# Optimization experiments

Measured on AMD Instinct MI355X. Metric: run time of the kernel, lower is better.

The kernel has to match this reference:

```python
import jax, jax.numpy as jnp
import numpy as np

H, W = 192, 640
MAX_ITERS = 200
EPS = 1e-8


def setup_inputs() -> dict:
    key = jax.random.key(0)
    k1, k2 = jax.random.split(key)
    B = 16
    ptcloud = jax.random.normal(k1, (B, 3, H * W), dtype=jnp.float32)
    # KITTI-like intrinsics; cy = 96 so the ground prior starts at row 96.
    Kmat = jnp.tile(
        jnp.array([[721.5, 0.0, 320.0], [0.0, 721.5, 96.0], [0.0, 0.0, 1.0]],
                  dtype=jnp.float32)[None], (B, 1, 1))
    ys = 96
    xs, xe = W * 3 // 8, W * 5 // 8
    n_prior = (H - ys) * (xe - xs)  # 15360
    sample_idx = jax.random.randint(k2, (MAX_ITERS, 3), 0, n_prior, dtype=jnp.int32)
    return {"ptcloud": ptcloud, "K": Kmat, "sample_idx": sample_idx}


def _median_low(x):
    """torch.median semantics (lower middle element), x: (B, N) -> (B, 1)."""
    n = x.shape[1]
    s = jnp.sort(x, axis=1)
    m = (n - 1) // 2
    return s[:, m:m + 1]


def _mad_threshold(y):
    med = _median_low(y)                       # (B, 1)
    return _median_low(jnp.abs(med - y))       # (B, 1)


def _ransac_plane(prior, sample_idx, thr):
    """prior: (B, N, 3), sample_idx: (I, 3), thr: (B, 1) -> plane (B, 4)."""
    samples = prior[:, sample_idx]             # (B, I, 3, 3)
    p1, p2, p3 = samples[:, :, 0], samples[:, :, 1], samples[:, :, 2]
    n = jnp.cross(p2 - p1, p3 - p1)            # (B, I, 3)
    n = n / (jnp.linalg.norm(n, axis=-1, keepdims=True) + EPS)
    d = -jnp.sum(n * p1, axis=-1)              # (B, I)
    # point-plane distances for all prior points: (B, I, N)
    dist = jnp.abs(jnp.einsum('bnc,bic->bin', prior, n) + d[:, :, None])
    counts = jnp.sum(dist <= thr[:, :, None], axis=-1)  # (B, I)
    best = jnp.argmax(counts, axis=1)                    # (B,)
    plane = jnp.concatenate([n, d[..., None]], axis=-1)  # (B, I, 4)
    return jnp.take_along_axis(plane, best[:, None, None], axis=1)[:, 0]


def reference(ptcloud, K, sample_idx):
    B = ptcloud.shape[0]
    # ground prior region (static slice; K is concrete at trace time here)
    ys = int(K[:, 1, 2].mean())
    xs, xe = W * 3 // 8, W * 5 // 8
    pc = ptcloud.reshape(B, 3, H, W)
    prior = pc[:, :, ys:, xs:xe].reshape(B, 3, -1).transpose(0, 2, 1)  # (B, N, 3)
    thr = _mad_threshold(prior[..., 1])                                # (B, 1)
    plane = _ransac_plane(prior, sample_idx, thr)                      # (B, 4)
    pts_all = ptcloud.transpose(0, 2, 1)                               # (B, M, 3)
    dist_all = jnp.abs(jnp.einsum('bmc,bc->bm', pts_all, plane[:, :3]) + plane[:, 3:4])
    inlier_mask = (dist_all <= thr).reshape(B, H, W)
    return plane, inlier_mask
```

## Files before the change

kernel.cpp:

```cpp
#include <hip/hip_runtime.h>
#include <cstdint>

#define HW      122880
#define NPRIOR  15360
#define NITER   200
#define NB      16
#define RANKSEL 7680u
#define NBINS   8192
#define LISTCAP 2048

__device__ __forceinline__ uint32_t f2k(float f) {
  uint32_t u = __float_as_uint(f);
  return (u & 0x80000000u) ? ~u : (u ^ 0x80000000u);
}
__device__ __forceinline__ float k2f(uint32_t k) {
  uint32_t u = (k & 0x80000000u) ? (k ^ 0x80000000u) : ~k;
  return __uint_as_float(u);
}

__device__ uint32_t select13(uint32_t* __restrict__ keys, uint32_t* __restrict__ hist,
                             uint32_t* __restrict__ wpart, uint32_t* __restrict__ res,
                             uint32_t* __restrict__ list, uint32_t* __restrict__ pcnt,
                             uint32_t* __restrict__ pfin, int tid) {
  {
    uint4 z = {0u, 0u, 0u, 0u};
    ((uint4*)hist)[tid] = z;
    ((uint4*)hist)[1024 + tid] = z;
  }
  if (tid == 0) *pcnt = 0u;
  __syncthreads();
#pragma unroll
  for (int j = 0; j < 15; j++) {
    uint32_t k = keys[j * 1024 + tid];
    atomicAdd(&hist[k >> 19], 1u);
  }
  __syncthreads();
  uint32_t h[8];
  uint32_t s = 0u;
#pragma unroll
  for (int e = 0; e < 8; e++) {
    h[e] = hist[8 * tid + e];
    s += h[e];
  }
  uint32_t incl = s;
#pragma unroll
  for (int off = 1; off < 64; off <<= 1) {
    uint32_t n = __shfl_up(incl, off);
    if ((tid & 63) >= off) incl += n;
  }
  if ((tid & 63) == 63) wpart[tid >> 6] = incl;
  __syncthreads();
  {
    uint32_t base = 0u;
    const int wv = tid >> 6;
#pragma unroll
    for (int w = 0; w < 16; w++) base += (w < wv) ? wpart[w] : 0u;
    incl += base;
  }
  const uint32_t excl = incl - s;
  if (RANKSEL > excl && RANKSEL <= incl) {
    uint32_t c = excl;
#pragma unroll
    for (int e = 0; e < 8; e++) {
      uint32_t nc = c + h[e];
      if (RANKSEL > c && RANKSEL <= nc) {
        res[0] = (uint32_t)(8 * tid + e);
        res[1] = RANKSEL - c;
      }
      c = nc;
    }
  }
  __syncthreads();
  const uint32_t bin = res[0];
  const uint32_t tp = res[1];
#pragma unroll
  for (int j = 0; j < 15; j++) {
    uint32_t k = keys[j * 1024 + tid];
    if ((k >> 19) == bin) {
      uint32_t p = atomicAdd(pcnt, 1u);
      if (p < LISTCAP) list[p] = k & 0x7FFFFu;
    }
  }
  __syncthreads();
  if (tid < 64) {
    const uint32_t n = *pcnt;
    uint32_t kk[8];
#pragma unroll
    for (int j = 0; j < 8; j++) {
      uint32_t p = (uint32_t)tid + 64u * j;
      kk[j] = (p < n) ? list[p] : 0xFFFFFFFFu;
    }
    uint32_t lo = 0u, hi = 0x7FFFFu;
    while (lo < hi) {
      uint32_t mid = lo + ((hi - lo) >> 1);
      int c = 0;
#pragma unroll
      for (int j = 0; j < 8; j++) c += (kk[j] <= mid) ? 1 : 0;
      for (uint32_t p = 512u + (uint32_t)tid; p < n; p += 64u)
        c += (list[p] <= mid) ? 1 : 0;
#pragma unroll
      for (int off = 32; off; off >>= 1) c += __shfl_down(c, off);
      c = __shfl(c, 0);
      if ((uint32_t)c >= tp) hi = mid; else lo = mid + 1u;
    }
    if (tid == 0) *pfin = (bin << 19) | lo;
  }
  __syncthreads();
  return *pfin;
}

__global__ __launch_bounds__(1024, 4)
void thr_kernel(const float* __restrict__ pt, const int* __restrict__ sidx,
                float* __restrict__ thr_out, float* __restrict__ planes,
                uint32_t* __restrict__ bestkey) {
  __shared__ uint32_t keys[NPRIOR];
  __shared__ uint32_t hist[NBINS];
  __shared__ uint32_t list[LISTCAP];
  __shared__ uint32_t wpart[16];
  __shared__ uint32_t res[2];
  __shared__ uint32_t lcnt;
  __shared__ uint32_t fin;
  const int b = blockIdx.x;
  const int tid = threadIdx.x;
  if (tid == 0) bestkey[b] = 0u;

  if (tid < NITER) {
    const float* base = pt + (size_t)b * 3 * HW;
    float p[3][3];
#pragma unroll
    for (int k = 0; k < 3; k++) {
      int s = sidx[tid * 3 + k];
      int r = s / 160;
      int c = s - r * 160;
      int hw = (96 + r) * 640 + 240 + c;
      p[k][0] = base[hw];
      p[k][1] = base[HW + hw];
      p[k][2] = base[2 * HW + hw];
    }
    float ux = __fsub_rn(p[1][0], p[0][0]);
    float uy = __fsub_rn(p[1][1], p[0][1]);
    float uz = __fsub_rn(p[1][2], p[0][2]);
    float vx = __fsub_rn(p[2][0], p[0][0]);
    float vy = __fsub_rn(p[2][1], p[0][1]);
    float vz = __fsub_rn(p[2][2], p[0][2]);
    float nx = __fsub_rn(__fmul_rn(uy, vz), __fmul_rn(uz, vy));
    float ny = __fsub_rn(__fmul_rn(uz, vx), __fmul_rn(ux, vz));
    float nz = __fsub_rn(__fmul_rn(ux, vy), __fmul_rn(uy, vx));
    float nn = __fsqrt_rn(__fadd_rn(__fadd_rn(__fmul_rn(nx, nx), __fmul_rn(ny, ny)),
                                    __fmul_rn(nz, nz)));
    float den = __fadd_rn(nn, 1e-8f);
    nx = __fdiv_rn(nx, den);
    ny = __fdiv_rn(ny, den);
    nz = __fdiv_rn(nz, den);
    float s3 = __fadd_rn(__fadd_rn(__fmul_rn(nx, p[0][0]), __fmul_rn(ny, p[0][1])),
                         __fmul_rn(nz, p[0][2]));
    int t = b * NITER + tid;
    planes[4 * t + 0] = nx;
    planes[4 * t + 1] = ny;
    planes[4 * t + 2] = nz;
    planes[4 * t + 3] = -s3;
  }

  const float* ybase = pt + (size_t)b * 3 * HW + HW;
#pragma unroll
  for (int j = 0; j < 15; j++) {
    int i = j * 1024 + tid;
    int r = i / 160;
    int c = i - r * 160;
    keys[j * 1024 + tid] = f2k(ybase[(96 + r) * 640 + 240 + c]);
  }
  uint32_t medk = select13(keys, hist, wpart, res, list, &lcnt, &fin, tid);
  float med = k2f(medk);

#pragma unroll
  for (int j = 0; j < 15; j++) {
    float y = k2f(keys[j * 1024 + tid]);
    keys[j * 1024 + tid] = __float_as_uint(fabsf(__fsub_rn(med, y)));
  }
  uint32_t thk = select13(keys, hist, wpart, res, list, &lcnt, &fin, tid);
  if (tid == 0) thr_out[b] = __uint_as_float(thk);
}

__global__ __launch_bounds__(256)
void count_kernel(const float* __restrict__ pt, const float* __restrict__ planes,
                  const float* __restrict__ thr_arr, uint32_t* __restrict__ bestkey) {
  const int chunk = blockIdx.x;
  const int b = blockIdx.y;
  const int tid = threadIdx.x;
  __shared__ int cnt_s[13];
  if (tid < 13) cnt_s[tid] = 0;
  __syncthreads();
  const int p0 = chunk * 13;
  float plr[13][4];
#pragma unroll
  for (int k = 0; k < 13; k++) {
    int pidx = p0 + k;
    if (pidx < NITER) {
      const float* pp = planes + (size_t)(b * NITER + pidx) * 4;
      plr[k][0] = pp[0]; plr[k][1] = pp[1]; plr[k][2] = pp[2]; plr[k][3] = pp[3];
    } else {
      plr[k][0] = plr[k][1] = plr[k][2] = plr[k][3] = 0.0f;
    }
  }
  const float thr = thr_arr[b];
  const float* base = pt + (size_t)b * 3 * HW;
  int cnt[13];
#pragma unroll
  for (int k = 0; k < 13; k++) cnt[k] = 0;
  for (int ii = 0; ii < NPRIOR; ii += 1024) {
    int i = ii + tid * 4;
    int r = i / 160;
    int c = i - r * 160;
    int hw = (96 + r) * 640 + 240 + c;
    float4 x4 = *(const float4*)(base + hw);
    float4 y4 = *(const float4*)(base + HW + hw);
    float4 z4 = *(const float4*)(base + 2 * HW + hw);
    float xs[4] = {x4.x, x4.y, x4.z, x4.w};
    float ys[4] = {y4.x, y4.y, y4.z, y4.w};
    float zs[4] = {z4.x, z4.y, z4.z, z4.w};
#pragma unroll
    for (int q = 0; q < 4; q++) {
      float x = xs[q], y = ys[q], z = zs[q];
#pragma unroll
      for (int k = 0; k < 13; k++) {
        float s = __fadd_rn(__fadd_rn(__fmul_rn(x, plr[k][0]), __fmul_rn(y, plr[k][1])),
                            __fmul_rn(z, plr[k][2]));
        float dist = fabsf(__fadd_rn(s, plr[k][3]));
        cnt[k] += (dist <= thr) ? 1 : 0;
      }
    }
  }
#pragma unroll
  for (int k = 0; k < 13; k++) {
    int v = cnt[k];
#pragma unroll
    for (int off = 32; off; off >>= 1) v += __shfl_down(v, off);
    if ((tid & 63) == 0) atomicAdd(&cnt_s[k], v);
  }
  __syncthreads();
  if (tid < 13 && p0 + tid < NITER) {
    int iter = p0 + tid;
    uint32_t key = ((uint32_t)cnt_s[tid] << 8) | (uint32_t)(255 - iter);
    atomicMax(&bestkey[b], key);
  }
}

__global__ __launch_bounds__(256)
void mask_kernel(const float* __restrict__ pt, const float* __restrict__ planes,
                 const float* __restrict__ thr_arr, const uint32_t* __restrict__ bestkey,
                 float* __restrict__ out) {
  const int g4 = (blockIdx.x * 256 + threadIdx.x) * 4;
  const int b = g4 / HW;
  const int m = g4 - b * HW;
  const int best = 255 - (int)(bestkey[b] & 255u);
  const float* plane = planes + (size_t)(b * NITER + best) * 4;
  const float nx = plane[0], ny = plane[1], nz = plane[2], dd = plane[3];
  const float thr = thr_arr[b];
  const float* base = pt + (size_t)b * 3 * HW;
  float4 x4 = *(const float4*)(base + m);
  float4 y4 = *(const float4*)(base + HW + m);
  float4 z4 = *(const float4*)(base + 2 * HW + m);
  float xs[4] = {x4.x, x4.y, x4.z, x4.w};
  float ys[4] = {y4.x, y4.y, y4.z, y4.w};
  float zs[4] = {z4.x, z4.y, z4.z, z4.w};
  float4 o;
  float* os = (float*)&o;
#pragma unroll
  for (int q = 0; q < 4; q++) {
    float s = __fadd_rn(__fadd_rn(__fmul_rn(xs[q], nx), __fmul_rn(ys[q], ny)),
                        __fmul_rn(zs[q], nz));
    float dist = fabsf(__fadd_rn(s, dd));
    os[q] = (dist <= thr) ? 1.0f : 0.0f;
  }
  *(float4*)(out + 64 + (size_t)g4) = o;
  if (m == 0) {
#pragma unroll
    for (int q = 0; q < 4; q++) out[b * 4 + q] = plane[q];
  }
}

extern "C" void kernel_launch(void* const* d_in, const int* in_sizes, int n_in,
                              void* d_out, int out_size, void* d_ws, size_t ws_size,
                              hipStream_t stream) {
  (void)in_sizes; (void)n_in; (void)out_size; (void)ws_size;
  const float* pt = (const float*)d_in[0];
  const int* sidx = (const int*)d_in[2];
  float* out = (float*)d_out;

  float* thr      = (float*)d_ws;
  float* planes   = thr + 16;
  uint32_t* bkey  = (uint32_t*)(planes + NB * NITER * 4);

  thr_kernel<<<NB, 1024, 0, stream>>>(pt, sidx, thr, planes, bkey);
  count_kernel<<<dim3(16, NB), 256, 0, stream>>>(pt, planes, thr, bkey);
  mask_kernel<<<(NB * HW) / 1024, 256, 0, stream>>>(pt, planes, thr, bkey, out);
}
```

Baseline: 119.0 us.

## Fuse threshold, count, and mask stages into one cooperative kernel with grid sync

Replaces the three separate launches with a single cooperative kernel of 256 blocks that uses grid-wide syncs between the threshold/plane stage, the RANSAC count stage and the mask stage. The median selection now runs with 256 threads and rereads y values from global memory instead of keeping keys in shared memory. Plane generation is spread across 200 blocks, with one plane per batch computed by each thread. The aim is to cut launch gaps and the serial tail of a 16-block threshold kernel, at the cost of grid.sync overhead and a threshold stage with fewer threads per batch.

```diff
diff --git a/kernel.cpp b/kernel.cpp
--- a/kernel.cpp
+++ b/kernel.cpp
@@ -1,5 +1,8 @@
 #include <hip/hip_runtime.h>
+#include <hip/hip_cooperative_groups.h>
 #include <cstdint>
+
+namespace cg = cooperative_groups;
 
 #define HW      122880
 #define NPRIOR  15360
@@ -18,29 +21,39 @@
   return __uint_as_float(u);
 }
 
-__device__ uint32_t select13(uint32_t* __restrict__ keys, uint32_t* __restrict__ hist,
-                             uint32_t* __restrict__ wpart, uint32_t* __restrict__ res,
-                             uint32_t* __restrict__ list, uint32_t* __restrict__ pcnt,
-                             uint32_t* __restrict__ pfin, int tid) {
+__device__ uint32_t select256(const float* __restrict__ ybase, int tid,
+                              bool pass2, float med, uint32_t* __restrict__ hist,
+                              uint32_t* __restrict__ list, uint32_t* __restrict__ wpart,
+                              uint32_t* __restrict__ res, uint32_t* __restrict__ pcnt,
+                              uint32_t* __restrict__ pfin) {
   {
     uint4 z = {0u, 0u, 0u, 0u};
-    ((uint4*)hist)[tid] = z;
-    ((uint4*)hist)[1024 + tid] = z;
+#pragma unroll
+    for (int j = 0; j < 8; j++) ((uint4*)hist)[tid + j * 256] = z;
   }
   if (tid == 0) *pcnt = 0u;
   __syncthreads();
 #pragma unroll
   for (int j = 0; j < 15; j++) {
-    uint32_t k = keys[j * 1024 + tid];
-    atomicAdd(&hist[k >> 19], 1u);
-  }
-  __syncthreads();
-  uint32_t h[8];
+    int i = tid * 4 + j * 1024;
+    int r = i / 160;
+    int c = i - r * 160;
+    float4 v = *(const float4*)(ybase + (96 + r) * 640 + 240 + c);
+    float vs[4] = {v.x, v.y, v.z, v.w};
+#pragma unroll
+    for (int e = 0; e < 4; e++) {
+      uint32_t k = pass2 ? __float_as_uint(fabsf(__fsub_rn(med, vs[e]))) : f2k(vs[e]);
+      atomicAdd(&hist[k >> 19], 1u);
+    }
+  }
+  __syncthreads();
+  uint32_t h[32];
   uint32_t s = 0u;
 #pragma unroll
-  for (int e = 0; e < 8; e++) {
-    h[e] = hist[8 * tid + e];
-    s += h[e];
+  for (int j = 0; j < 8; j++) {
+    uint4 q = ((const uint4*)hist)[8 * tid + j];
+    h[4 * j + 0] = q.x; h[4 * j + 1] = q.y; h[4 * j + 2] = q.z; h[4 * j + 3] = q.w;
+    s += q.x + q.y + q.z + q.w;
   }
   uint32_t incl = s;
 #pragma unroll
@@ -54,17 +67,17 @@
     uint32_t base = 0u;
     const int wv = tid >> 6;
 #pragma unroll
-    for (int w = 0; w < 16; w++) base += (w < wv) ? wpart[w] : 0u;
+    for (int w = 0; w < 4; w++) base += (w < wv) ? wpart[w] : 0u;
     incl += base;
   }
   const uint32_t excl = incl - s;
   if (RANKSEL > excl && RANKSEL <= incl) {
     uint32_t c = excl;
 #pragma unroll
-    for (int e = 0; e < 8; e++) {
+    for (int e = 0; e < 32; e++) {
       uint32_t nc = c + h[e];
       if (RANKSEL > c && RANKSEL <= nc) {
-        res[0] = (uint32_t)(8 * tid + e);
+        res[0] = (uint32_t)(32 * tid + e);
         res[1] = RANKSEL - c;
       }
       c = nc;
@@ -75,10 +88,18 @@
   const uint32_t tp = res[1];
 #pragma unroll
   for (int j = 0; j < 15; j++) {
-    uint32_t k = keys[j * 1024 + tid];
-    if ((k >> 19) == bin) {
-      uint32_t p = atomicAdd(pcnt, 1u);
-      if (p < LISTCAP) list[p] = k & 0x7FFFFu;
+    int i = tid * 4 + j * 1024;
+    int r = i / 160;
+    int c = i - r * 160;
+    float4 v = *(const float4*)(ybase + (96 + r) * 640 + 240 + c);
+    float vs[4] = {v.x, v.y, v.z, v.w};
+#pragma unroll
+    for (int e = 0; e < 4; e++) {
+      uint32_t k = pass2 ? __float_as_uint(fabsf(__fsub_rn(med, vs[e]))) : f2k(vs[e]);
+      if ((k >> 19) == bin) {
+        uint32_t p = atomicAdd(pcnt, 1u);
+        if (p < LISTCAP) list[p] = k & 0x7FFFFu;
+      }
     }
   }
   __syncthreads();
@@ -109,173 +130,163 @@
   return *pfin;
 }
 
-__global__ __launch_bounds__(1024, 4)
-void thr_kernel(const float* __restrict__ pt, const int* __restrict__ sidx,
-                float* __restrict__ thr_out, float* __restrict__ planes,
-                uint32_t* __restrict__ bestkey) {
-  __shared__ uint32_t keys[NPRIOR];
+__global__ __launch_bounds__(256)
+void fused_kernel(const float* __restrict__ pt, const int* __restrict__ sidx,
+                  float* __restrict__ thr_arr, float* __restrict__ planes,
+                  uint32_t* __restrict__ bestkey, float* __restrict__ out) {
   __shared__ uint32_t hist[NBINS];
   __shared__ uint32_t list[LISTCAP];
-  __shared__ uint32_t wpart[16];
+  __shared__ uint32_t wpart[4];
   __shared__ uint32_t res[2];
-  __shared__ uint32_t lcnt;
-  __shared__ uint32_t fin;
-  const int b = blockIdx.x;
+  __shared__ uint32_t pcnt, pfin;
+  __shared__ int cnt_s[13];
+  cg::grid_group grid = cg::this_grid();
+  const int g = blockIdx.x;
   const int tid = threadIdx.x;
-  if (tid == 0) bestkey[b] = 0u;
-
-  if (tid < NITER) {
+
+  if (g < NB) {
+    const int b = g;
+    const float* ybase = pt + (size_t)b * 3 * HW + HW;
+    uint32_t medk = select256(ybase, tid, false, 0.0f, hist, list, wpart, res, &pcnt, &pfin);
+    float med = k2f(medk);
+    uint32_t thk = select256(ybase, tid, true, med, hist, list, wpart, res, &pcnt, &pfin);
+    if (tid == 0) thr_arr[b] = __uint_as_float(thk);
+  } else if (g < 16 + NITER) {
+    const int i = g - 16;
+    if (tid < NB) {
+      const int b = tid;
+      const float* base = pt + (size_t)b * 3 * HW;
+      float p[3][3];
+#pragma unroll
+      for (int k = 0; k < 3; k++) {
+        int s = sidx[i * 3 + k];
+        int r = s / 160;
+        int c = s - r * 160;
+        int hw = (96 + r) * 640 + 240 + c;
+        p[k][0] = base[hw];
+        p[k][1] = base[HW + hw];
+        p[k][2] = base[2 * HW + hw];
+      }
+      float ux = __fsub_rn(p[1][0], p[0][0]);
+      float uy = __fsub_rn(p[1][1], p[0][1]);
+      float uz = __fsub_rn(p[1][2], p[0][2]);
+      float vx = __fsub_rn(p[2][0], p[0][0]);
+      float vy = __fsub_rn(p[2][1], p[0][1]);
+      float vz = __fsub_rn(p[2][2], p[0][2]);
+      float nx = __fsub_rn(__fmul_rn(uy, vz), __fmul_rn(uz, vy));
+      float ny = __fsub_rn(__fmul_rn(uz, vx), __fmul_rn(ux, vz));
+      float nz = __fsub_rn(__fmul_rn(ux, vy), __fmul_rn(uy, vx));
+      float nn = __fsqrt_rn(__fadd_rn(__fadd_rn(__fmul_rn(nx, nx), __fmul_rn(ny, ny)),
+                                      __fmul_rn(nz, nz)));
+      float den = __fadd_rn(nn, 1e-8f);
+      nx = __fdiv_rn(nx, den);
+      ny = __fdiv_rn(ny, den);
+      nz = __fdiv_rn(nz, den);
+      float s3 = __fadd_rn(__fadd_rn(__fmul_rn(nx, p[0][0]), __fmul_rn(ny, p[0][1])),
+                           __fmul_rn(nz, p[0][2]));
+      int t = b * NITER + i;
+      planes[4 * t + 0] = nx;
+      planes[4 * t + 1] = ny;
+      planes[4 * t + 2] = nz;
+      planes[4 * t + 3] = -s3;
+    }
+  } else if (g == 16 + NITER) {
+    if (tid < NB) bestkey[tid] = 0u;
+  }
+  grid.sync();
+
+  {
+    const int b = g >> 4;
+    const int chunk = g & 15;
+    if (tid < 13) cnt_s[tid] = 0;
+    __syncthreads();
+    const int p0 = chunk * 13;
+    float plr[13][4];
+#pragma unroll
+    for (int k = 0; k < 13; k++) {
+      int pidx = p0 + k;
+      if (pidx < NITER) {
+        const float* pp = planes + (size_t)(b * NITER + pidx) * 4;
+        plr[k][0] = pp[0]; plr[k][1] = pp[1]; plr[k][2] = pp[2]; plr[k][3] = pp[3];
+      } else {
+        plr[k][0] = plr[k][1] = plr[k][2] = plr[k][3] = 0.0f;
+      }
+    }
+    const float thr = thr_arr[b];
     const float* base = pt + (size_t)b * 3 * HW;
-    float p[3][3];
-#pragma unroll
-    for (int k = 0; k < 3; k++) {
-      int s = sidx[tid * 3 + k];
-      int r = s / 160;
-      int c = s - r * 160;
+    int cnt[13];
+#pragma unroll
+    for (int k = 0; k < 13; k++) cnt[k] = 0;
+    for (int ii = 0; ii < NPRIOR; ii += 1024) {
+      int i = ii + tid * 4;
+      int r = i / 160;
+      int c = i - r * 160;
       int hw = (96 + r) * 640 + 240 + c;
-      p[k][0] = base[hw];
-      p[k][1] = base[HW + hw];
-      p[k][2] = base[2 * HW + hw];
-    }
-    float ux = __fsub_rn(p[1][0], p[0][0]);
-    float uy = __fsub_rn(p[1][1], p[0][1]);
-    float uz = __fsub_rn(p[1][2], p[0][2]);
-    float vx = __fsub_rn(p[2][0], p[0][0]);
-    float vy = __fsub_rn(p[2][1], p[0][1]);
-    float vz = __fsub_rn(p[2][2], p[0][2]);
-    float nx = __fsub_rn(__fmul_rn(uy, vz), __fmul_rn(uz, vy));
-    float ny = __fsub_rn(__fmul_rn(uz, vx), __fmul_rn(ux, vz));
-    float nz = __fsub_rn(__fmul_rn(ux, vy), __fmul_rn(uy, vx));
-    float nn = __fsqrt_rn(__fadd_rn(__fadd_rn(__fmul_rn(nx, nx), __fmul_rn(ny, ny)),
-                                    __fmul_rn(nz, nz)));
-    float den = __fadd_rn(nn, 1e-8f);
-    nx = __fdiv_rn(nx, den);
-    ny = __fdiv_rn(ny, den);
-    nz = __fdiv_rn(nz, den);
-    float s3 = __fadd_rn(__fadd_rn(__fmul_rn(nx, p[0][0]), __fmul_rn(ny, p[0][1])),
-                         __fmul_rn(nz, p[0][2]));
-    int t = b * NITER + tid;
-    planes[4 * t + 0] = nx;
-    planes[4 * t + 1] = ny;
-    planes[4 * t + 2] = nz;
-    planes[4 * t + 3] = -s3;
-  }
-
-  const float* ybase = pt + (size_t)b * 3 * HW + HW;
-#pragma unroll
-  for (int j = 0; j < 15; j++) {
-    int i = j * 1024 + tid;
-    int r = i / 160;
-    int c = i - r * 160;
-    keys[j * 1024 + tid] = f2k(ybase[(96 + r) * 640 + 240 + c]);
-  }
-  uint32_t medk = select13(keys, hist, wpart, res, list, &lcnt, &fin, tid);
-  float med = k2f(medk);
-
-#pragma unroll
-  for (int j = 0; j < 15; j++) {
-    float y = k2f(keys[j * 1024 + tid]);
-    keys[j * 1024 + tid] = __float_as_uint(fabsf(__fsub_rn(med, y)));
-  }
-  uint32_t thk = select13(keys, hist, wpart, res, list, &lcnt, &fin, tid);
-  if (tid == 0) thr_out[b] = __uint_as_float(thk);
-}
-
-__global__ __launch_bounds__(256)
-void count_kernel(const float* __restrict__ pt, const float* __restrict__ planes,
-                  const float* __restrict__ thr_arr, uint32_t* __restrict__ bestkey) {
-  const int chunk = blockIdx.x;
-  const int b = blockIdx.y;
-  const int tid = threadIdx.x;
-  __shared__ int cnt_s[13];
-  if (tid < 13) cnt_s[tid] = 0;
-  __syncthreads();
-  const int p0 = chunk * 13;
-  float plr[13][4];
-#pragma unroll
-  for (int k = 0; k < 13; k++) {
-    int pidx = p0 + k;
-    if (pidx < NITER) {
-      const float* pp = planes + (size_t)(b * NITER + pidx) * 4;
-      plr[k][0] = pp[0]; plr[k][1] = pp[1]; plr[k][2] = pp[2]; plr[k][3] = pp[3];
-    } else {
-      plr[k][0] = plr[k][1] = plr[k][2] = plr[k][3] = 0.0f;
-    }
-  }
-  const float thr = thr_arr[b];
-  const float* base = pt + (size_t)b * 3 * HW;
-  int cnt[13];
-#pragma unroll
-  for (int k = 0; k < 13; k++) cnt[k] = 0;
-  for (int ii = 0; ii < NPRIOR; ii += 1024) {
-    int i = ii + tid * 4;
-    int r = i / 160;
-    int c = i - r * 160;
-    int hw = (96 + r) * 640 + 240 + c;
-    float4 x4 = *(const float4*)(base + hw);
-    float4 y4 = *(const float4*)(base + HW + hw);
-    float4 z4 = *(const float4*)(base + 2 * HW + hw);
+      float4 x4 = *(const float4*)(base + hw);
+      float4 y4 = *(const float4*)(base + HW + hw);
+      float4 z4 = *(const float4*)(base + 2 * HW + hw);
+      float xs[4] = {x4.x, x4.y, x4.z, x4.w};
+      float ys[4] = {y4.x, y4.y, y4.z, y4.w};
+      float zs[4] = {z4.x, z4.y, z4.z, z4.w};
+#pragma unroll
+      for (int q = 0; q < 4; q++) {
+        float x = xs[q], y = ys[q], z = zs[q];
+#pragma unroll
+        for (int k = 0; k < 13; k++) {
+          float s = __fadd_rn(__fadd_rn(__fmul_rn(x, plr[k][0]), __fmul_rn(y, plr[k][1])),
+                              __fmul_rn(z, plr[k][2]));
+          float dist = fabsf(__fadd_rn(s, plr[k][3]));
+          cnt[k] += (dist <= thr) ? 1 : 0;
+        }
+      }
+    }
+#pragma unroll
+    for (int k = 0; k < 13; k++) {
+      int v = cnt[k];
+#pragma unroll
+      for (int off = 32; off; off >>= 1) v += __shfl_down(v, off);
+      if ((tid & 63) == 0) atomicAdd(&cnt_s[k], v);
+    }
+    __syncthreads();
+    if (tid < 13 && p0 + tid < NITER) {
+      int iter = p0 + tid;
+      uint32_t key = ((uint32_t)cnt_s[tid] << 8) | (uint32_t)(255 - iter);
+      atomicMax(&bestkey[b], key);
+    }
+  }
+  grid.sync();
+
+  for (uint32_t u = (uint32_t)g * 256u + (uint32_t)tid; u < (uint32_t)(NB * HW / 4);
+       u += 65536u) {
+    const int g4 = (int)u * 4;
+    const int b = g4 / HW;
+    const int m = g4 - b * HW;
+    const int best = 255 - (int)(bestkey[b] & 255u);
+    const float* plane = planes + (size_t)(b * NITER + best) * 4;
+    const float nx = plane[0], ny = plane[1], nz = plane[2], dd = plane[3];
+    const float thr = thr_arr[b];
+    const float* base = pt + (size_t)b * 3 * HW;
+    float4 x4 = *(const float4*)(base + m);
+    float4 y4 = *(const float4*)(base + HW + m);
+    float4 z4 = *(const float4*)(base + 2 * HW + m);
     float xs[4] = {x4.x, x4.y, x4.z, x4.w};
     float ys[4] = {y4.x, y4.y, y4.z, y4.w};
     float zs[4] = {z4.x, z4.y, z4.z, z4.w};
+    float4 o;
+    float* os = (float*)&o;
 #pragma unroll
     for (int q = 0; q < 4; q++) {
-      float x = xs[q], y = ys[q], z = zs[q];
-#pragma unroll
-      for (int k = 0; k < 13; k++) {
-        float s = __fadd_rn(__fadd_rn(__fmul_rn(x, plr[k][0]), __fmul_rn(y, plr[k][1])),
-                            __fmul_rn(z, plr[k][2]));
-        float dist = fabsf(__fadd_rn(s, plr[k][3]));
-        cnt[k] += (dist <= thr) ? 1 : 0;
-      }
-    }
-  }
-#pragma unroll
-  for (int k = 0; k < 13; k++) {
-    int v = cnt[k];
-#pragma unroll
-    for (int off = 32; off; off >>= 1) v += __shfl_down(v, off);
-    if ((tid & 63) == 0) atomicAdd(&cnt_s[k], v);
-  }
-  __syncthreads();
-  if (tid < 13 && p0 + tid < NITER) {
-    int iter = p0 + tid;
-    uint32_t key = ((uint32_t)cnt_s[tid] << 8) | (uint32_t)(255 - iter);
-    atomicMax(&bestkey[b], key);
-  }
-}
-
-__global__ __launch_bounds__(256)
-void mask_kernel(const float* __restrict__ pt, const float* __restrict__ planes,
-                 const float* __restrict__ thr_arr, const uint32_t* __restrict__ bestkey,
-                 float* __restrict__ out) {
-  const int g4 = (blockIdx.x * 256 + threadIdx.x) * 4;
-  const int b = g4 / HW;
-  const int m = g4 - b * HW;
-  const int best = 255 - (int)(bestkey[b] & 255u);
-  const float* plane = planes + (size_t)(b * NITER + best) * 4;
-  const float nx = plane[0], ny = plane[1], nz = plane[2], dd = plane[3];
-  const float thr = thr_arr[b];
-  const float* base = pt + (size_t)b * 3 * HW;
-  float4 x4 = *(const float4*)(base + m);
-  float4 y4 = *(const float4*)(base + HW + m);
-  float4 z4 = *(const float4*)(base + 2 * HW + m);
-  float xs[4] = {x4.x, x4.y, x4.z, x4.w};
-  float ys[4] = {y4.x, y4.y, y4.z, y4.w};
-  float zs[4] = {z4.x, z4.y, z4.z, z4.w};
-  float4 o;
-  float* os = (float*)&o;
-#pragma unroll
-  for (int q = 0; q < 4; q++) {
-    float s = __fadd_rn(__fadd_rn(__fmul_rn(xs[q], nx), __fmul_rn(ys[q], ny)),
-                        __fmul_rn(zs[q], nz));
-    float dist = fabsf(__fadd_rn(s, dd));
-    os[q] = (dist <= thr) ? 1.0f : 0.0f;
-  }
-  *(float4*)(out + 64 + (size_t)g4) = o;
-  if (m == 0) {
-#pragma unroll
-    for (int q = 0; q < 4; q++) out[b * 4 + q] = plane[q];
+      float s = __fadd_rn(__fadd_rn(__fmul_rn(xs[q], nx), __fmul_rn(ys[q], ny)),
+                          __fmul_rn(zs[q], nz));
+      float dist = fabsf(__fadd_rn(s, dd));
+      os[q] = (dist <= thr) ? 1.0f : 0.0f;
+    }
+    *(float4*)(out + 64 + (size_t)g4) = o;
+  }
+  if (g == 0 && tid < 64) {
+    const int b = tid >> 2;
+    const int best = 255 - (int)(bestkey[b] & 255u);
+    out[tid] = planes[(size_t)(b * NITER + best) * 4 + (tid & 3)];
   }
 }
 
@@ -291,7 +302,8 @@
   float* planes   = thr + 16;
   uint32_t* bkey  = (uint32_t*)(planes + NB * NITER * 4);
 
-  thr_kernel<<<NB, 1024, 0, stream>>>(pt, sidx, thr, planes, bkey);
-  count_kernel<<<dim3(16, NB), 256, 0, stream>>>(pt, planes, thr, bkey);
-  mask_kernel<<<(NB * HW) / 1024, 256, 0, stream>>>(pt, planes, thr, bkey, out);
-}
+  void* args[] = {(void*)&pt, (void*)&sidx, (void*)&thr, (void*)&planes,
+                  (void*)&bkey, (void*)&out};
+  hipLaunchCooperativeKernel((const void*)fused_kernel, dim3(256), dim3(256),
+                             args, 0, stream);
+}
```

Result: slower. 193.9 us (+62.9%).
